# Performance work log

Hardware: AMD Instinct MI355X
Metric: run time of the kernel (lower is better)

The kernel has to match this reference:

```python
import jax, jax.numpy as jnp
import numpy as np

N = 50000        # num nodes
E = 800000       # num edges (before self loops)
IN = 256         # in_channels
H = 4            # heads
C = 32           # out_channels per head
NEG_SLOPE = 0.2


def _glorot(key, shape):
    fan = shape[-2] * (shape[-1] if len(shape) > 2 else 1) + shape[-1]
    # PyG glorot: uniform(-s, s) with s = sqrt(6 / (fan_in + fan_out))
    s = float(np.sqrt(6.0 / (shape[-2] + shape[-1])))
    return jax.random.uniform(key, shape, jnp.float32, -s, s)


def setup_inputs() -> dict:
    key = jax.random.key(0)
    k1, k2, k3, k4, k5 = jax.random.split(key, 5)
    x = jax.random.normal(k1, (N, IN), jnp.float32)
    src = jax.random.randint(k2, (E,), 0, N)
    dst = jax.random.randint(k3, (E,), 0, N)
    # guarantee no self loops (module removes them then re-adds exactly N loops)
    dst = jnp.where(dst == src, (dst + 1) % N, dst)
    edge_index = jnp.stack([src, dst]).astype(jnp.int32)
    weight = _glorot(k4, (IN, H * C))
    att = _glorot(k5, (1, H, 2 * C))
    bias = jnp.zeros((H * C,), jnp.float32)
    return {"x": x, "weight": weight, "att": att, "bias": bias,
            "edge_index": edge_index}


def reference(x, weight, att, bias, edge_index):
    n = x.shape[0]
    # linear projection -> [N, H, C]
    h = (x @ weight).reshape(n, H, C)
    # add self loops (input edge_index has none)
    loops = jnp.arange(n, dtype=edge_index.dtype)
    ei = jnp.concatenate([edge_index, jnp.stack([loops, loops])], axis=1)
    src, dst = ei[0], ei[1]          # flow source_to_target: j=src(row 0), i=dst(row 1)
    x_j = h[src]                     # [E', H, C] source features
    x_i = h[dst]                     # [E', H, C] target features
    wl = att[:, :, :C]               # applied to x_i (first half of concat)
    wr = att[:, :, C:]               # applied to x_j
    alpha = (x_i * wl).sum(-1) + (x_j * wr).sum(-1)   # [E', H]
    alpha = jax.nn.leaky_relu(alpha, NEG_SLOPE)
    # NOTE: module normalizes softmax over edge_index[0] (src) segments
    seg = src
    amax = jax.ops.segment_max(alpha, seg, num_segments=n)
    alpha = jnp.exp(alpha - amax[seg])
    denom = jax.ops.segment_sum(alpha, seg, num_segments=n)
    alpha = alpha / (denom[seg] + 1e-16)
    # weighted messages, aggregated at edge_index[i] = edge_index[1] (dst)
    msg = x_j * alpha[:, :, None]                     # [E', H, C]
    out = jax.ops.segment_sum(msg, dst, num_segments=n)  # [N, H, C]
    return out.reshape(n, H * C) + bias
```

## Files before the change

kernel.cpp:

```cpp
#include <hip/hip_runtime.h>
#include <hip/hip_fp16.h>
#include <math.h>


#define NH 4
#define CH 32
#define HC 128
#define IND 256
#define NEG_SLOPE 0.2f
#define CSH 8
#define NCB_MAX 256
#define CHUNK 4096
#define BCAP 6144

typedef __attribute__((ext_vector_type(8))) short bf16x8;
typedef __attribute__((ext_vector_type(16))) float f32x16;

__device__ __forceinline__ unsigned short f2bf(float f) {
    unsigned int u = __float_as_uint(f);
    unsigned int r = (u + 0x7FFFu + ((u >> 16) & 1u)) >> 16;
    return (unsigned short)r;
}
__device__ __forceinline__ float bf2f(unsigned short s) {
    return __uint_as_float(((unsigned int)s) << 16);
}

__global__ __launch_bounds__(256) void k_wprep(const float* __restrict__ W,
                                               unsigned short* __restrict__ WT_bf,
                                               int* __restrict__ gcurS,
                                               int* __restrict__ gcurD) {
    int t = blockIdx.x * 256 + threadIdx.x;
    if (blockIdx.x == 0) { gcurS[threadIdx.x] = 0; gcurD[threadIdx.x] = 0; }
    if (t < IND * HC) {
        int c = t >> 8;
        int k = t & 255;
        WT_bf[t] = f2bf(W[k * HC + c]);
    }
}

__global__ __launch_bounds__(512) void k_gs(const float* __restrict__ x,
                                            const unsigned short* __restrict__ WT_bf,
                                            const float* __restrict__ att,
                                            unsigned short* __restrict__ h_bf,
                                            float* __restrict__ al,
                                            float* __restrict__ ar,
                                            const int* __restrict__ ei,
                                            int* __restrict__ gcurS,
                                            int* __restrict__ gcurD,
                                            unsigned int* __restrict__ recS,
                                            unsigned int* __restrict__ recD,
                                            int E, int NE, int ncb, int nsb, int N) {
    __shared__ float cs[128 * 132];

    const int tid = threadIdx.x;

    if (blockIdx.x < nsb) {
        unsigned int* srt = (unsigned int*)cs;
        int* cnt  = (int*)(srt + CHUNK);
        int* off  = cnt + NCB_MAX;
        int* cur  = off + NCB_MAX;
        int* gpos = cur + NCB_MAX;
        int* sc   = gpos + NCB_MAX;

        const int t0 = blockIdx.x * CHUNK;
        const int m  = min(CHUNK, NE - t0);

        unsigned int myrec[CHUNK / 512];
        int nmy = 0;
        for (int i = tid; i < m; i += 512) {
            int t = t0 + i;
            int src, dst;
            if (t < E) { src = ei[t]; dst = ei[E + t]; }
            else       { src = dst = t - E; }
            myrec[nmy++] = (unsigned int)src | ((unsigned int)dst << 16);
        }

        for (int side = 0; side < 2; side++) {
            if (tid < 256) cnt[tid] = 0;
            __syncthreads();
            int mybkt[CHUNK / 512];
            for (int k = 0; k < nmy; k++) {
                unsigned int r = myrec[k];
                int node = side ? (int)(r >> 16) : (int)(r & 0xFFFFu);
                mybkt[k] = node >> CSH;
                atomicAdd(&cnt[mybkt[k]], 1);
            }
            __syncthreads();
            int v = (tid < 256) ? cnt[tid] : 0;
            if (tid < 256) sc[tid] = v;
            __syncthreads();
            for (int o = 1; o < 256; o <<= 1) {
                int t = (tid >= o && tid < 256) ? sc[tid - o] : 0;
                __syncthreads();
                if (tid < 256) sc[tid] += t;
                __syncthreads();
            }
            if (tid < 256) { off[tid] = sc[tid] - v; cur[tid] = sc[tid] - v; }
            __syncthreads();
            for (int k = 0; k < nmy; k++) {
                int p = atomicAdd(&cur[mybkt[k]], 1);
                srt[p] = myrec[k];
            }
            __syncthreads();
            int* gcur = side ? gcurD : gcurS;
            if (tid < ncb) {
                int c = cnt[tid];
                gpos[tid] = c ? atomicAdd(&gcur[tid], c) : 0;
            }
            __syncthreads();
            unsigned int* recX = side ? recD : recS;
            for (int i = tid; i < m; i += 512) {
                unsigned int r = srt[i];
                int node = side ? (int)(r >> 16) : (int)(r & 0xFFFFu);
                int cb = node >> CSH;
                int p  = gpos[cb] + (i - off[cb]);
                if (p < BCAP)
                    recX[(size_t)cb * BCAP + p] = r;
            }
            __syncthreads();
        }
        return;
    }

    unsigned short* wsT = (unsigned short*)cs;

    const int row0 = (blockIdx.x - nsb) * 256;
    const int wave = tid >> 6;
    const int lane = tid & 63;
    const int n32  = lane & 31;
    const int half = lane >> 5;

    {
        int c  = tid >> 2;
        int kq = (tid & 3) * 64;
        const unsigned short* src = WT_bf + c * IND + kq;
        unsigned short* dst = wsT + c * 258 + kq;
#pragma unroll
        for (int j = 0; j < 64; j += 8)
            *(int4*)(dst + j) = *(const int4*)(src + j);
    }
    __syncthreads();

    const int row   = row0 + wave * 32 + n32;
    const bool valid = row < N;
    const float* xrow = x + (size_t)row * IND + half * 8;

    f32x16 acc[4];
#pragma unroll
    for (int t = 0; t < 4; t++)
#pragma unroll
        for (int r = 0; r < 16; r++) acc[t][r] = 0.0f;

#pragma unroll 4
    for (int s = 0; s < 16; s++) {
        float4 v0 = make_float4(0.f, 0.f, 0.f, 0.f);
        float4 v1 = v0;
        if (valid) {
            v0 = *(const float4*)(xrow + s * 16);
            v1 = *(const float4*)(xrow + s * 16 + 4);
        }
        bf16x8 a;
        a[0] = (short)f2bf(v0.x); a[1] = (short)f2bf(v0.y);
        a[2] = (short)f2bf(v0.z); a[3] = (short)f2bf(v0.w);
        a[4] = (short)f2bf(v1.x); a[5] = (short)f2bf(v1.y);
        a[6] = (short)f2bf(v1.z); a[7] = (short)f2bf(v1.w);
#pragma unroll
        for (int t = 0; t < 4; t++) {
            bf16x8 b = *(const bf16x8*)(wsT + (t * 32 + n32) * 258 + s * 16 + half * 8);
            acc[t] = __builtin_amdgcn_mfma_f32_32x32x16_bf16(a, b, acc[t], 0, 0, 0);
        }
    }
    __syncthreads();

    for (int pass = 0; pass < 2; pass++) {
        if ((wave >> 2) == pass) {
            const int lw = wave & 3;
#pragma unroll
            for (int t = 0; t < 4; t++)
#pragma unroll
                for (int r = 0; r < 16; r++) {
                    int rl = lw * 32 + (r & 3) + 8 * (r >> 2) + 4 * half;
                    cs[rl * 132 + t * 33 + n32] = acc[t][r];
                }
        }
        __syncthreads();

        const int rl   = tid >> 2;
        const int hq   = tid & 3;
        const int orow = row0 + pass * 128 + rl;
        if (orow < N) {
            const float* cr = cs + rl * 132 + hq * 33;
            unsigned short* hp = h_bf + (size_t)orow * HC + hq * CH;
#pragma unroll
            for (int c = 0; c < 32; c += 8) {
                ushort4 o0, o1;
                o0.x = f2bf(cr[c]);     o0.y = f2bf(cr[c + 1]);
                o0.z = f2bf(cr[c + 2]); o0.w = f2bf(cr[c + 3]);
                o1.x = f2bf(cr[c + 4]); o1.y = f2bf(cr[c + 5]);
                o1.z = f2bf(cr[c + 6]); o1.w = f2bf(cr[c + 7]);
                *(ushort4*)(hp + c) = o0;
                *(ushort4*)(hp + c + 4) = o1;
            }
            const float* w0 = att + hq * (2 * CH);
            float sl = 0.f, sr = 0.f;
#pragma unroll
            for (int c = 0; c < CH; c++) {
                float v = cr[c];
                sl += v * w0[c];
                sr += v * w0[CH + c];
            }
            al[orow * NH + hq] = sl;
            ar[orow * NH + hq] = sr;
        }
        __syncthreads();
    }
}

__global__ __launch_bounds__(256) void k_bucket(const unsigned int* __restrict__ recS,
                                                const unsigned int* __restrict__ recD,
                                                const int* __restrict__ gcurS,
                                                const int* __restrict__ gcurD,
                                                const float* __restrict__ al,
                                                const float* __restrict__ ar,
                                                unsigned short* __restrict__ adjD,
                                                int* __restrict__ rowB,
                                                int* __restrict__ rowE,
                                                float* __restrict__ arw,
                                                int ncb, int N) {
    __shared__ int cnt[256], cur[256], sc[256];
    __shared__ float lsums[256 * NH];
    __shared__ float lar[256 * NH];
    const int tid = threadIdx.x;

    if (blockIdx.x < ncb) {
        const int cb = blockIdx.x;
        const int b0 = cb * BCAP;
        const int tot_rec = min(gcurD[cb], BCAP);

        cnt[tid] = 0;
        __syncthreads();
        for (int i = tid; i < tot_rec; i += 256) {
            unsigned int r = recD[b0 + i];
            atomicAdd(&cnt[(r >> 16) & 255], 1);
        }
        __syncthreads();
        int v = cnt[tid];
        sc[tid] = v;
        __syncthreads();
        for (int o = 1; o < 256; o <<= 1) {
            int t = (tid >= o) ? sc[tid - o] : 0;
            __syncthreads();
            sc[tid] += t;
            __syncthreads();
        }
        int ex = sc[tid] - v;
        int node_g = (cb << CSH) + tid;
        if (node_g < N) { rowB[node_g] = b0 + ex; rowE[node_g] = b0 + ex + v; }
        cur[tid] = ex;
        __syncthreads();
        for (int i = tid; i < tot_rec; i += 256) {
            unsigned int r = recD[b0 + i];
            int node = (int)(r >> 16) & 255;
            int p = atomicAdd(&cur[node], 1);
            adjD[b0 + p] = (unsigned short)(r & 0xFFFFu);
        }
    } else {
        const int cb = blockIdx.x - ncb;
        const int b0 = cb * BCAP;
        const int b1 = b0 + min(gcurS[cb], BCAP);
        const int node_g = (cb << CSH) + tid;

        float4 arv = make_float4(0.f, 0.f, 0.f, 0.f);
        if (node_g < N) arv = *(const float4*)(ar + (size_t)node_g * NH);
        *(float4*)(lar + tid * NH) = arv;
        *(float4*)(lsums + tid * NH) = make_float4(0.f, 0.f, 0.f, 0.f);
        __syncthreads();

        int i = b0 + tid;
        for (; i + 256 < b1; i += 512) {
            unsigned int r0 = recS[i];
            unsigned int r1 = recS[i + 256];
            int sl0 = (int)(r0 & 255u), dst0 = (int)(r0 >> 16);
            int sl1 = (int)(r1 & 255u), dst1 = (int)(r1 >> 16);
            float4 av0 = *(const float4*)(al + (size_t)dst0 * NH);
            float4 av1 = *(const float4*)(al + (size_t)dst1 * NH);
            const float* w0 = lar + sl0 * NH;
            const float* w1 = lar + sl1 * NH;
            float a0 = av0.x + w0[0], a1 = av0.y + w0[1];
            float a2 = av0.z + w0[2], a3 = av0.w + w0[3];
            float c0 = av1.x + w1[0], c1 = av1.y + w1[1];
            float c2 = av1.z + w1[2], c3 = av1.w + w1[3];
            a0 = (a0 > 0.f) ? a0 : NEG_SLOPE * a0;
            a1 = (a1 > 0.f) ? a1 : NEG_SLOPE * a1;
            a2 = (a2 > 0.f) ? a2 : NEG_SLOPE * a2;
            a3 = (a3 > 0.f) ? a3 : NEG_SLOPE * a3;
            c0 = (c0 > 0.f) ? c0 : NEG_SLOPE * c0;
            c1 = (c1 > 0.f) ? c1 : NEG_SLOPE * c1;
            c2 = (c2 > 0.f) ? c2 : NEG_SLOPE * c2;
            c3 = (c3 > 0.f) ? c3 : NEG_SLOPE * c3;
            float* s0 = lsums + sl0 * NH;
            float* s1 = lsums + sl1 * NH;
            atomicAdd(s0 + 0, __expf(a0));
            atomicAdd(s0 + 1, __expf(a1));
            atomicAdd(s0 + 2, __expf(a2));
            atomicAdd(s0 + 3, __expf(a3));
            atomicAdd(s1 + 0, __expf(c0));
            atomicAdd(s1 + 1, __expf(c1));
            atomicAdd(s1 + 2, __expf(c2));
            atomicAdd(s1 + 3, __expf(c3));
        }
        if (i < b1) {
            unsigned int r = recS[i];
            int slot = (int)(r & 255u);
            int dst  = (int)(r >> 16);
            float4 alv = *(const float4*)(al + (size_t)dst * NH);
            const float* av = lar + slot * NH;
            float a0 = alv.x + av[0], a1 = alv.y + av[1];
            float a2 = alv.z + av[2], a3 = alv.w + av[3];
            a0 = (a0 > 0.f) ? a0 : NEG_SLOPE * a0;
            a1 = (a1 > 0.f) ? a1 : NEG_SLOPE * a1;
            a2 = (a2 > 0.f) ? a2 : NEG_SLOPE * a2;
            a3 = (a3 > 0.f) ? a3 : NEG_SLOPE * a3;
            float* sp = lsums + slot * NH;
            atomicAdd(sp + 0, __expf(a0));
            atomicAdd(sp + 1, __expf(a1));
            atomicAdd(sp + 2, __expf(a2));
            atomicAdd(sp + 3, __expf(a3));
        }
        __syncthreads();

        if (node_g < N) {
            const float* sp = lsums + tid * NH;
            float4 p0 = make_float4(arv.x, 1.0f / (sp[0] + 1e-16f),
                                    arv.y, 1.0f / (sp[1] + 1e-16f));
            float4 p1 = make_float4(arv.z, 1.0f / (sp[2] + 1e-16f),
                                    arv.w, 1.0f / (sp[3] + 1e-16f));
            *(float4*)(arw + (size_t)node_g * 8)     = p0;
            *(float4*)(arw + (size_t)node_g * 8 + 4) = p1;
        }
    }
}

__global__ __launch_bounds__(256) void k_agg(const int* __restrict__ rowB,
                                             const int* __restrict__ rowE,
                                             const unsigned short* __restrict__ adjD,
                                             const float* __restrict__ al,
                                             const float* __restrict__ arw,
                                             const unsigned short* __restrict__ h_bf,
                                             const float* __restrict__ bias,
                                             float* __restrict__ out, int N) {
    const int g = threadIdx.x >> 5;
    const int n = blockIdx.x * 8 + g;
    if (n >= N) return;
    const int l  = threadIdx.x & 31;
    const int c0 = l * 4;
    const int hh = l >> 3;
    const int beg = rowB[n], end = rowE[n];
    const float alv = al[n * NH + hh];

    float a0 = 0.f, a1 = 0.f, a2 = 0.f, a3 = 0.f;

    for (int base = beg; base < end; base += 32) {
        int idx = base + l;
        int av  = (idx < end) ? (int)adjD[idx] : 0;
        int cnt = min(32, end - base);
        int e = 0;
        for (; e + 4 <= cnt; e += 4) {
            int s0 = __shfl(av, e,     32);
            int s1 = __shfl(av, e + 1, 32);
            int s2 = __shfl(av, e + 2, 32);
            int s3 = __shfl(av, e + 3, 32);
            ushort4 u0 = *(const ushort4*)(h_bf + (size_t)s0 * HC + c0);
            ushort4 u1 = *(const ushort4*)(h_bf + (size_t)s1 * HC + c0);
            ushort4 u2 = *(const ushort4*)(h_bf + (size_t)s2 * HC + c0);
            ushort4 u3 = *(const ushort4*)(h_bf + (size_t)s3 * HC + c0);
            float2 p0 = *(const float2*)(arw + (size_t)s0 * 8 + hh * 2);
            float2 p1 = *(const float2*)(arw + (size_t)s1 * 8 + hh * 2);
            float2 p2 = *(const float2*)(arw + (size_t)s2 * 8 + hh * 2);
            float2 p3 = *(const float2*)(arw + (size_t)s3 * 8 + hh * 2);
            float t0 = alv + p0.x; t0 = (t0 > 0.f) ? t0 : NEG_SLOPE * t0;
            float t1 = alv + p1.x; t1 = (t1 > 0.f) ? t1 : NEG_SLOPE * t1;
            float t2 = alv + p2.x; t2 = (t2 > 0.f) ? t2 : NEG_SLOPE * t2;
            float t3 = alv + p3.x; t3 = (t3 > 0.f) ? t3 : NEG_SLOPE * t3;
            float w0 = __expf(t0) * p0.y;
            float w1 = __expf(t1) * p1.y;
            float w2 = __expf(t2) * p2.y;
            float w3 = __expf(t3) * p3.y;
            a0 += bf2f(u0.x) * w0; a1 += bf2f(u0.y) * w0;
            a2 += bf2f(u0.z) * w0; a3 += bf2f(u0.w) * w0;
            a0 += bf2f(u1.x) * w1; a1 += bf2f(u1.y) * w1;
            a2 += bf2f(u1.z) * w1; a3 += bf2f(u1.w) * w1;
            a0 += bf2f(u2.x) * w2; a1 += bf2f(u2.y) * w2;
            a2 += bf2f(u2.z) * w2; a3 += bf2f(u2.w) * w2;
            a0 += bf2f(u3.x) * w3; a1 += bf2f(u3.y) * w3;
            a2 += bf2f(u3.z) * w3; a3 += bf2f(u3.w) * w3;
        }
        for (; e < cnt; e++) {
            int s0 = __shfl(av, e, 32);
            ushort4 u0 = *(const ushort4*)(h_bf + (size_t)s0 * HC + c0);
            float2 p0 = *(const float2*)(arw + (size_t)s0 * 8 + hh * 2);
            float t0 = alv + p0.x; t0 = (t0 > 0.f) ? t0 : NEG_SLOPE * t0;
            float w0 = __expf(t0) * p0.y;
            a0 += bf2f(u0.x) * w0; a1 += bf2f(u0.y) * w0;
            a2 += bf2f(u0.z) * w0; a3 += bf2f(u0.w) * w0;
        }
    }
    float4 b4 = *(const float4*)(bias + c0);
    *(float4*)(out + (size_t)n * HC + c0) =
        make_float4(a0 + b4.x, a1 + b4.y, a2 + b4.z, a3 + b4.w);
}

extern "C" void kernel_launch(void* const* d_in, const int* in_sizes, int n_in,
                              void* d_out, int out_size, void* d_ws, size_t ws_size,
                              hipStream_t stream) {
    const float* x    = (const float*)d_in[0];
    const float* W    = (const float*)d_in[1];
    const float* att  = (const float*)d_in[2];
    const float* bias = (const float*)d_in[3];
    const int*   ei   = (const int*)d_in[4];

    const int N  = in_sizes[0] / IND;
    const int E  = in_sizes[4] / 2;
    const int NE = E + N;
    const int ncb = (N + (1 << CSH) - 1) >> CSH;
    const int nsb = (NE + CHUNK - 1) / CHUNK;
    const int ngb = (N + 255) / 256;
    float* out = (float*)d_out;
    const int nodeTot = N * NH;
    const size_t capTot = (size_t)ncb * BCAP;

    unsigned short* h_bf  = (unsigned short*)d_ws;
    unsigned short* WT_bf = h_bf + (size_t)N * HC;
    float* al   = (float*)(WT_bf + IND * HC);
    float* ar   = al + nodeTot;
    float* arw  = ar + nodeTot;
    unsigned int* recS = (unsigned int*)(arw + (size_t)N * 8);
    unsigned int* recD = recS + capTot;
    unsigned short* adjD = (unsigned short*)(recD + capTot);
    int* rowB    = (int*)(adjD + capTot + (capTot & 1));
    int* rowE    = rowB + N;
    int* gcurS   = rowE + N;
    int* gcurD   = gcurS + NCB_MAX;

    k_wprep<<<(IND * HC + 255) / 256, 256, 0, stream>>>(W, WT_bf, gcurS, gcurD);
    k_gs<<<nsb + ngb, 512, 0, stream>>>(x, WT_bf, att, h_bf, al, ar, ei,
                                        gcurS, gcurD, recS, recD,
                                        E, NE, ncb, nsb, N);
    k_bucket<<<2 * ncb, 256, 0, stream>>>(recS, recD, gcurS, gcurD, al, ar,
                                          adjD, rowB, rowE, arw, ncb, N);
    k_agg<<<(N + 7) / 8, 256, 0, stream>>>(rowB, rowE, adjD, al, arw, h_bf,
                                           bias, out, N);
}
```

Before: 204.9 us.

## Stage x tiles through double-buffered LDS and put GEMM blocks first

The GEMM part of the fused gemm/scatter kernel now loads x with coalesced float4 reads across the block, converts it to bf16, and stages it in two LDS buffers in 64-column panels. The next panel's global load overlaps the MFMA work on the current one. Block ordering is also swapped so GEMM blocks launch before the edge-sort blocks. The cost is more shared memory per block (about 135KB), which may cut occupancy to one block per CU.

```diff
diff --git a/kernel.cpp b/kernel.cpp
--- a/kernel.cpp
+++ b/kernel.cpp
@@ -49,20 +49,20 @@
                                             int* __restrict__ gcurD,
                                             unsigned int* __restrict__ recS,
                                             unsigned int* __restrict__ recD,
-                                            int E, int NE, int ncb, int nsb, int N) {
-    __shared__ float cs[128 * 132];
+                                            int E, int NE, int ncb, int ngb, int N) {
+    __shared__ __align__(16) unsigned short smem[67840];
 
     const int tid = threadIdx.x;
 
-    if (blockIdx.x < nsb) {
-        unsigned int* srt = (unsigned int*)cs;
+    if (blockIdx.x >= ngb) {
+        unsigned int* srt = (unsigned int*)smem;
         int* cnt  = (int*)(srt + CHUNK);
         int* off  = cnt + NCB_MAX;
         int* cur  = off + NCB_MAX;
         int* gpos = cur + NCB_MAX;
         int* sc   = gpos + NCB_MAX;
 
-        const int t0 = blockIdx.x * CHUNK;
+        const int t0 = (blockIdx.x - ngb) * CHUNK;
         const int m  = min(CHUNK, NE - t0);
 
         unsigned int myrec[CHUNK / 512];
@@ -122,9 +122,11 @@
         return;
     }
 
-    unsigned short* wsT = (unsigned short*)cs;
-
-    const int row0 = (blockIdx.x - nsb) * 256;
+    unsigned short* xs0 = smem;
+    unsigned short* xs1 = smem + 17408;
+    unsigned short* wsT = smem + 34816;
+
+    const int row0 = blockIdx.x * 256;
     const int wave = tid >> 6;
     const int lane = tid & 63;
     const int n32  = lane & 31;
@@ -139,39 +141,66 @@
         for (int j = 0; j < 64; j += 8)
             *(int4*)(dst + j) = *(const int4*)(src + j);
     }
+
+    float4 v[8];
+#define STAGE_LOAD(p)                                                        \
+    {                                                                        \
+        _Pragma("unroll")                                                    \
+        for (int j = 0; j < 8; j++) {                                        \
+            int fid = j * 512 + tid;                                         \
+            int gr  = row0 + (fid >> 4);                                     \
+            float4 t = make_float4(0.f, 0.f, 0.f, 0.f);                      \
+            if (gr < N)                                                      \
+                t = *(const float4*)(x + (size_t)gr * IND + (p) * 64 +       \
+                                     (fid & 15) * 4);                        \
+            v[j] = t;                                                        \
+        }                                                                    \
+    }
+#define STAGE_WRITE(buf)                                                     \
+    {                                                                        \
+        _Pragma("unroll")                                                    \
+        for (int j = 0; j < 8; j++) {                                        \
+            int fid = j * 512 + tid;                                         \
+            int row = fid >> 4;                                              \
+            ushort4 o;                                                       \
+            o.x = f2bf(v[j].x); o.y = f2bf(v[j].y);                          \
+            o.z = f2bf(v[j].z); o.w = f2bf(v[j].w);                          \
+            *(ushort4*)((buf) + row * 68 + (fid & 15) * 4) = o;              \
+        }                                                                    \
+    }
+
+    STAGE_LOAD(0);
+    STAGE_WRITE(xs0);
     __syncthreads();
 
-    const int row   = row0 + wave * 32 + n32;
-    const bool valid = row < N;
-    const float* xrow = x + (size_t)row * IND + half * 8;
-
     f32x16 acc[4];
 #pragma unroll
     for (int t = 0; t < 4; t++)
 #pragma unroll
         for (int r = 0; r < 16; r++) acc[t][r] = 0.0f;
 
-#pragma unroll 4
-    for (int s = 0; s < 16; s++) {
-        float4 v0 = make_float4(0.f, 0.f, 0.f, 0.f);
-        float4 v1 = v0;
-        if (valid) {
-            v0 = *(const float4*)(xrow + s * 16);
-            v1 = *(const float4*)(xrow + s * 16 + 4);
-        }
-        bf16x8 a;
-        a[0] = (short)f2bf(v0.x); a[1] = (short)f2bf(v0.y);
-        a[2] = (short)f2bf(v0.z); a[3] = (short)f2bf(v0.w);
-        a[4] = (short)f2bf(v1.x); a[5] = (short)f2bf(v1.y);
-        a[6] = (short)f2bf(v1.z); a[7] = (short)f2bf(v1.w);
-#pragma unroll
-        for (int t = 0; t < 4; t++) {
-            bf16x8 b = *(const bf16x8*)(wsT + (t * 32 + n32) * 258 + s * 16 + half * 8);
-            acc[t] = __builtin_amdgcn_mfma_f32_32x32x16_bf16(a, b, acc[t], 0, 0, 0);
-        }
-    }
-    __syncthreads();
-
+    const int arow = wave * 32 + n32;
+#pragma unroll
+    for (int p = 0; p < 4; p++) {
+        if (p < 3) STAGE_LOAD(p + 1);
+        const unsigned short* xb = (p & 1) ? xs1 : xs0;
+#pragma unroll
+        for (int s = 0; s < 4; s++) {
+            bf16x8 a = *(const bf16x8*)(xb + arow * 68 + s * 16 + half * 8);
+#pragma unroll
+            for (int t = 0; t < 4; t++) {
+                bf16x8 b = *(const bf16x8*)(wsT + (t * 32 + n32) * 258 +
+                                            p * 64 + s * 16 + half * 8);
+                acc[t] = __builtin_amdgcn_mfma_f32_32x32x16_bf16(a, b, acc[t], 0, 0, 0);
+            }
+        }
+        if (p < 3) STAGE_WRITE((p & 1) ? xs0 : xs1);
+        __syncthreads();
+    }
+#undef STAGE_LOAD
+#undef STAGE_WRITE
+
+    float* cs = (float*)smem;
     for (int pass = 0; pass < 2; pass++) {
         if ((wave >> 2) == pass) {
             const int lw = wave & 3;
@@ -205,9 +234,9 @@
             float sl = 0.f, sr = 0.f;
 #pragma unroll
             for (int c = 0; c < CH; c++) {
-                float v = cr[c];
-                sl += v * w0[c];
-                sr += v * w0[CH + c];
+                float v2 = cr[c];
+                sl += v2 * w0[c];
+                sr += v2 * w0[CH + c];
             }
             al[orow * NH + hq] = sl;
             ar[orow * NH + hq] = sr;
@@ -443,9 +472,9 @@
     int* gcurD   = gcurS + NCB_MAX;
 
     k_wprep<<<(IND * HC + 255) / 256, 256, 0, stream>>>(W, WT_bf, gcurS, gcurD);
-    k_gs<<<nsb + ngb, 512, 0, stream>>>(x, WT_bf, att, h_bf, al, ar, ei,
+    k_gs<<<ngb + nsb, 512, 0, stream>>>(x, WT_bf, att, h_bf, al, ar, ei,
                                         gcurS, gcurD, recS, recD,
-                                        E, NE, ncb, nsb, N);
+                                        E, NE, ncb, ngb, N);
     k_bucket<<<2 * ncb, 256, 0, stream>>>(recS, recD, gcurS, gcurD, al, ar,
                                           adjD, rowB, rowE, arw, ncb, N);
     k_agg<<<(N + 7) / 8, 256, 0, stream>>>(rowB, rowE, adjD, al, arw, h_bf,
```

Result: slower. 212.9 us (+3.9%).
